# Optimization experiments

Hardware: AMD Instinct MI355X
Metric: run time of the kernel (lower is better)

Reference implementation:

```python
import jax, jax.numpy as jnp
import numpy as np
from jax import lax

STRIDE = 8  # backbone patch-embed stride


def setup_inputs() -> dict:
    key = jax.random.key(0)
    ks = jax.random.split(key, 5)
    B, H, W = 2, 256, 256
    Cr, Cg, Cout = 256, 5, 256
    N = 65536  # memory bank size
    return {
        "image": jax.random.normal(ks[0], (B, 3, H, W), dtype=jnp.float32),
        "geometry_map": jax.random.uniform(ks[1], (B, Cg, H, W), dtype=jnp.float32),
        "backbone_w": jax.random.normal(ks[2], (Cr, 3, STRIDE, STRIDE), dtype=jnp.float32) * 0.05,
        "backbone_b": jnp.zeros((Cr,), dtype=jnp.float32),
        "fusion_w": jax.random.normal(ks[3], (Cout, Cr + Cg), dtype=jnp.float32) * 0.05,
        "fusion_b": jnp.zeros((Cout,), dtype=jnp.float32),
        "memory_bank": jax.random.normal(ks[4], (N, Cout), dtype=jnp.float32),
    }


def reference(image, geometry_map, backbone_w, backbone_b, fusion_w, fusion_b, memory_bank):
    # --- backbone: patch-embed conv + relu -> (B,Cr,H',W') ---
    feat_rgb = lax.conv_general_dilated(
        image, backbone_w, window_strides=(STRIDE, STRIDE), padding="VALID",
        dimension_numbers=("NCHW", "OIHW", "NCHW"))
    feat_rgb = jax.nn.relu(feat_rgb + backbone_b[None, :, None, None])
    B, Cr, H, W = feat_rgb.shape

    # --- bilinear align of geometry map (align_corners=False semantics) ---
    geo = jax.image.resize(geometry_map, (B, geometry_map.shape[1], H, W), method="bilinear")

    # --- fusion 1x1 conv ---
    fused = jnp.concatenate([feat_rgb, geo], axis=1)           # (B, Cr+Cg, H, W)
    fused = jnp.einsum("oc,bchw->bohw", fusion_w, fused) + fusion_b[None, :, None, None]
    C = fused.shape[1]

    # --- NN min-distance to memory bank (cdist + min) ---
    flat = fused.transpose(0, 2, 3, 1).reshape(-1, C)          # (M, C)
    d2 = (jnp.sum(flat * flat, axis=1)[:, None]
          + jnp.sum(memory_bank * memory_bank, axis=1)[None, :]
          - 2.0 * flat @ memory_bank.T)                        # (M, N)
    min_dist = jnp.sqrt(jnp.maximum(jnp.min(d2, axis=1), 0.0))  # sqrt monotone: min before sqrt
    score_plain = min_dist.reshape(B, H, W)

    # --- geometry reweighting (sigmoid mode, alpha=1.0) ---
    density, opacity, anis = geo[:, 3:4], geo[:, 2:3], geo[:, 4:5]
    base = 0.5 * density + 0.25 * (1.0 - opacity) + 0.25 * anis
    w = 1.0 + jax.nn.sigmoid(4.0 * (base - 0.5))               # (B,1,H,W)
    score_geo = score_plain * w[:, 0]
    return score_plain, score_geo
```

## Files before the change

### kernel.cpp

```cpp
#include <hip/hip_runtime.h>
#include <hip/hip_bf16.h>
#include <stdint.h>

typedef __attribute__((ext_vector_type(8))) short bf16x8;
typedef __attribute__((ext_vector_type(4))) float f32x4;

#define NP 2048
#define NBANK 65536
#define NCHUNKS 32
#define CHUNK 2048
#define SUBR 64
#define NSUB 32
#define CF 261

__device__ inline short f2bf(float f) {
  __hip_bfloat16 h = __float2bfloat16(f);
  return *reinterpret_cast<short*>(&h);
}

__global__ __launch_bounds__(256) void k_repack_fw(
    const float* __restrict__ fw, float* __restrict__ fwp)
{
  int idx = blockIdx.x * 256 + threadIdx.x;
  int o = idx / 264, c = idx % 264;
  fwp[idx] = (c < CF) ? fw[(size_t)o * CF + c] : 0.f;
}

__global__ __launch_bounds__(512) void k_prep(
    const float* __restrict__ image, const float* __restrict__ geometry,
    const float* __restrict__ bw, const float* __restrict__ bb,
    const float* __restrict__ fwp, const float* __restrict__ fb,
    const float* __restrict__ mb,
    short* __restrict__ flatb, float* __restrict__ qsq, float* __restrict__ wgt,
    short* __restrict__ mbb, float* __restrict__ msq)
{
  __shared__ __align__(16) unsigned char shmem[32768];
  int t = threadIdx.x;
  int bid = blockIdx.x;

  if (bid >= 256) {
    int s = bid - 256;
    int r = t >> 3, q = t & 7;
    int wcs = r >> 5, hh = (r >> 4) & 1, l15r = r & 15;
    const float* src = mb + ((size_t)s * 64 + r) * 256;
    float s2 = 0.f;
    #pragma unroll
    for (int i = 0; i < 8; i++) {
      float4 v = *(const float4*)(src + q * 4 + i * 32);
      short4 o; o.x = f2bf(v.x); o.y = f2bf(v.y); o.z = f2bf(v.z); o.w = f2bf(v.w);
      int kbyte = q * 8 + i * 64;
      int ks = kbyte >> 6, l4 = (kbyte >> 4) & 3, b8 = kbyte & 8;
      int c = wcs * 16 + hh * 8 + ks;
      *(short4*)(shmem + c * 1024 + l4 * 256 + l15r * 16 + b8) = o;
      s2 += v.x * v.x + v.y * v.y + v.z * v.z + v.w * v.w;
    }
    s2 += __shfl_xor(s2, 1); s2 += __shfl_xor(s2, 2); s2 += __shfl_xor(s2, 4);
    if (q == 0) msq[(size_t)s * 64 + r] = s2;
    __syncthreads();
    unsigned char* dstg = (unsigned char*)mbb + (size_t)s * 32768;
    #pragma unroll
    for (int i = 0; i < 4; i++) {
      int S = t + i * 512;
      *(float4*)(dstg + S * 16) = *(const float4*)(shmem + S * 16);
    }
    return;
  }

  float* patch = (float*)shmem;
  float (*fusedS)[264] = (float (*)[264])(shmem + 6144);
  float (*gv)[8] = (float (*)[8])(shmem + 14592);
  float (*gw)[8] = (float (*)[8])(shmem + 15872);
  float (*redS)[8] = (float (*)[8])(shmem + 17152);

  int b = bid >> 7, rem = bid & 127, h = rem >> 2, w0 = (rem & 3) * 8;

  #pragma unroll
  for (int j = 0; j < 3; j++) {
    int idx = t + j * 512;
    int c = idx >> 9, r = (idx >> 6) & 7, col = idx & 63;
    patch[idx] = image[(((size_t)(b*3 + c) * 256) + 8*h + r) * 256 + 8*w0 + col];
  }
  if (t >= 320 && t < 344) {
    int i = (t - 320) / 3, c = 261 + (t - 320) % 3;
    fusedS[i][c] = 0.f;
  }
  if (t < 320) {
    int v = t >> 3, sub = t & 7;
    int i = v / 5, cg = v % 5;
    int jj = w0 + i;
    float val = 0.f, ws = 0.f;
    const float* gch = geometry + (size_t)(b*5 + cg) * 65536;
    #pragma unroll
    for (int rr = 0; rr < 2; rr++) {
      int r = sub * 2 + rr;
      int gr = 8*h - 4 + r;
      float wr = 1.f - fabsf((float)r - 7.5f) * 0.125f;
      if (gr >= 0 && gr < 256) {
        const float* grow = gch + (size_t)gr * 256;
        for (int c = 0; c < 16; c++) {
          int gc = 8*jj - 4 + c;
          if (gc >= 0 && gc < 256) {
            float wc_ = 1.f - fabsf((float)c - 7.5f) * 0.125f;
            val += wr * wc_ * grow[gc];
            ws  += wr * wc_;
          }
        }
      }
    }
    gv[v][sub] = val; gw[v][sub] = ws;
  }
  __syncthreads();
  if (t < 40) {
    int i = t / 5, cg = t % 5;
    float sv = 0.f, sw = 0.f;
    #pragma unroll
    for (int u = 0; u < 8; u++) { sv += gv[t][u]; sw += gw[t][u]; }
    fusedS[i][256 + cg] = sv / sw;
  }

  int g = t >> 8, o = t & 255;
  float a4[4] = {0.f, 0.f, 0.f, 0.f};
  const float4* wo4 = (const float4*)(bw + (size_t)o * 192);
  for (int cr = 0; cr < 24; cr++) {
    const float4* prow4 = (const float4*)&patch[cr * 64 + g * 32];
    float4 wA = wo4[cr*2], wB = wo4[cr*2 + 1];
    #pragma unroll
    for (int i4 = 0; i4 < 4; i4++) {
      float4 p0 = prow4[i4*2], p1 = prow4[i4*2 + 1];
      a4[i4] += wA.x*p0.x + wA.y*p0.y + wA.z*p0.z + wA.w*p0.w
              + wB.x*p1.x + wB.y*p1.y + wB.z*p1.z + wB.w*p1.w;
    }
  }
  float bias = bb[o];
  #pragma unroll
  for (int i4 = 0; i4 < 4; i4++) fusedS[g*4 + i4][o] = fmaxf(a4[i4] + bias, 0.f);
  __syncthreads();

  #pragma unroll
  for (int i4 = 0; i4 < 4; i4++) a4[i4] = 0.f;
  const float4* fwo4 = (const float4*)(fwp + (size_t)o * 264);
  for (int c4 = 0; c4 < 66; c4++) {
    float4 w4 = fwo4[c4];
    #pragma unroll
    for (int i4 = 0; i4 < 4; i4++) {
      float4 f4 = *(const float4*)&fusedS[g*4 + i4][c4*4];
      a4[i4] += w4.x*f4.x + w4.y*f4.y + w4.z*f4.z + w4.w*f4.w;
    }
  }
  float fbias = fb[o];
  int lane = t & 63, wid = t >> 6;
  #pragma unroll
  for (int i4 = 0; i4 < 4; i4++) {
    a4[i4] += fbias;
    int p = b*1024 + h*32 + w0 + g*4 + i4;
    flatb[(size_t)p * 256 + o] = f2bf(a4[i4]);
    float s = a4[i4] * a4[i4];
    #pragma unroll
    for (int m = 1; m < 64; m <<= 1) s += __shfl_xor(s, m);
    if (lane == 0) redS[g*4 + i4][wid & 3] = s;
  }
  __syncthreads();
  if (t < 8) {
    float s = redS[t][0] + redS[t][1] + redS[t][2] + redS[t][3];
    int p = b*1024 + h*32 + w0 + t;
    qsq[p] = s;
    float den = fusedS[t][256+3], opa = fusedS[t][256+2], ani = fusedS[t][256+4];
    float base2 = 0.5f*den + 0.25f*(1.f - opa) + 0.25f*ani;
    wgt[p] = 1.f + 1.f/(1.f + expf(-4.f*(base2 - 0.5f)));
  }
}

__global__ __launch_bounds__(256, 2) void k_distmin(
    const short* __restrict__ Aq, const short* __restrict__ Bb,
    const float* __restrict__ qsq, const float* __restrict__ msq,
    float* __restrict__ partial)
{
  __shared__ __align__(16) unsigned char sB[2][32768];
  __shared__ float red[2][128];
  int t = threadIdx.x;
  int lane = t & 63, wid = t >> 6;
  int wr = wid >> 1, wc = wid & 1;
  const int l15 = lane & 15, l4 = lane >> 4;
  int nc = blockIdx.x, mt = blockIdx.y;
  int m0 = mt * 128;
  const size_t nchunk0 = (size_t)nc * CHUNK;
  const unsigned char* Bbyte = (const unsigned char*)Bb + nchunk0 * 512;
  const unsigned char* Abyte = (const unsigned char*)Aq;

  bf16x8 af[4][8];
  #pragma unroll
  for (int mi = 0; mi < 4; mi++)
    #pragma unroll
    for (int ks = 0; ks < 8; ks++)
      af[mi][ks] = *(const bf16x8*)(Abyte +
          (size_t)(m0 + wr*64 + mi*16 + l15) * 512 + ks*64 + l4*16);

  float vmin[4][4];
  #pragma unroll
  for (int mi = 0; mi < 4; mi++)
    #pragma unroll
    for (int r = 0; r < 4; r++) vmin[mi][r] = 3.4e38f;

#define STAGE(bufsel, sidx) do {                                              \
    const unsigned char* gb_ = Bbyte + (size_t)(sidx) * 32768 + wid * 1024 + lane * 16; \
    unsigned char* lb_ = &sB[bufsel][0] + wid * 1024;                         \
    _Pragma("unroll")                                                         \
    for (int j_ = 0; j_ < 8; j_++) {                                          \
      __builtin_amdgcn_global_load_lds(                                       \
        (const __attribute__((address_space(1))) unsigned int*)(gb_ + j_*4096), \
        (__attribute__((address_space(3))) unsigned int*)(lb_ + j_*4096),     \
        16, 0, 0);                                                            \
    }                                                                         \
  } while (0)

  STAGE(0, 0);
  __syncthreads();

  int cur = 0;
  for (int s = 0; s < NSUB; s++) {
    if (s + 1 < NSUB) STAGE(cur ^ 1, s + 1);
    const size_t nb = nchunk0 + (size_t)s * SUBR;
    float msq0 = msq[nb + wc * 32 + l15];
    float msq1 = msq[nb + wc * 32 + 16 + l15];
    const unsigned char* buf = &sB[cur][0] + wc * 16384;

    f32x4 acc[4][2];
    #pragma unroll
    for (int mi = 0; mi < 4; mi++) {
      acc[mi][0] = (f32x4){0.f, 0.f, 0.f, 0.f};
      acc[mi][1] = (f32x4){0.f, 0.f, 0.f, 0.f};
    }
    #pragma unroll
    for (int ks = 0; ks < 8; ks++) {
      bf16x8 b0 = *(const bf16x8*)(buf + ks*1024 + l4*256 + l15*16);
      bf16x8 b1 = *(const bf16x8*)(buf + 8192 + ks*1024 + l4*256 + l15*16);
      #pragma unroll
      for (int mi = 0; mi < 4; mi++) {
        acc[mi][0] = __builtin_amdgcn_mfma_f32_16x16x32_bf16(af[mi][ks], b0, acc[mi][0], 0, 0, 0);
        acc[mi][1] = __builtin_amdgcn_mfma_f32_16x16x32_bf16(af[mi][ks], b1, acc[mi][1], 0, 0, 0);
      }
    }
    #pragma unroll
    for (int mi = 0; mi < 4; mi++)
      #pragma unroll
      for (int r = 0; r < 4; r++) {
        float v = fminf(msq0 - 2.f*acc[mi][0][r], msq1 - 2.f*acc[mi][1][r]);
        vmin[mi][r] = fminf(vmin[mi][r], v);
      }
    __syncthreads();
    cur ^= 1;
  }
#undef STAGE

  #pragma unroll
  for (int mi = 0; mi < 4; mi++)
    #pragma unroll
    for (int r = 0; r < 4; r++) {
      float v = vmin[mi][r];
      v = fminf(v, __shfl_xor(v, 1));
      v = fminf(v, __shfl_xor(v, 2));
      v = fminf(v, __shfl_xor(v, 4));
      v = fminf(v, __shfl_xor(v, 8));
      if (l15 == 0) red[wc][wr * 64 + mi * 16 + l4 * 4 + r] = v;
    }
  __syncthreads();
  if (t < 128) {
    float v = fminf(red[0][t], red[1][t]);
    float d2 = qsq[m0 + t] + v;
    partial[(size_t)(m0 + t) * NCHUNKS + nc] = fmaxf(d2, 0.f);
  }
}

__global__ __launch_bounds__(256) void k_final(
    const float* __restrict__ partial, const float* __restrict__ wgt,
    float* __restrict__ out)
{
  int q = blockIdx.x * 256 + threadIdx.x;
  const float4* p = (const float4*)(partial + (size_t)q * NCHUNKS);
  float v = 3.4e38f;
  #pragma unroll
  for (int j = 0; j < 8; j++) {
    float4 x = p[j];
    v = fminf(v, fminf(fminf(x.x, x.y), fminf(x.z, x.w)));
  }
  float sp = sqrtf(v);
  out[q] = sp;
  out[NP + q] = sp * wgt[q];
}

extern "C" void kernel_launch(void* const* d_in, const int* in_sizes, int n_in,
                              void* d_out, int out_size, void* d_ws, size_t ws_size,
                              hipStream_t stream) {
  const float* image    = (const float*)d_in[0];
  const float* geometry = (const float*)d_in[1];
  const float* bw       = (const float*)d_in[2];
  const float* bb       = (const float*)d_in[3];
  const float* fw       = (const float*)d_in[4];
  const float* fb       = (const float*)d_in[5];
  const float* mb       = (const float*)d_in[6];
  float* out = (float*)d_out;
  char* ws = (char*)d_ws;

  float* wgt     = (float*)(ws);
  float* qsq     = (float*)(ws + 8192);
  float* msq     = (float*)(ws + 16384);
  float* fwp     = (float*)(ws + 278528);
  short* flatb   = (short*)(ws + 548864);
  float* partial = (float*)(ws + 1597440);
  short* mbb     = (short*)(ws + 1859584);

  hipLaunchKernelGGL(k_repack_fw, dim3(264),     dim3(256), 0, stream, fw, fwp);
  hipLaunchKernelGGL(k_prep,      dim3(1280),    dim3(512), 0, stream,
                     image, geometry, bw, bb, fwp, fb, mb, flatb, qsq, wgt, mbb, msq);
  hipLaunchKernelGGL(k_distmin,   dim3(32, 16),  dim3(256), 0, stream, flatb, mbb, qsq, msq, partial);
  hipLaunchKernelGGL(k_final,     dim3(8),       dim3(256), 0, stream, partial, wgt, out);
}
```

Measured before the change: 199.2 us.

## Fuse prep, distmin and final stages into one cooperative persistent kernel

Merges the conv/fusion prep, memory-bank repack, distance-min and final reduction into a single cooperative kernel of 512 blocks separated by grid-wide syncs. A strided 2D device memcpy replaces the weight repack kernel. The conv blocks move to 256 threads, each producing all 8 pixels per output channel, and bank repack blocks handle 4 subtiles each. The goal is to remove kernel launch gaps and tail effects between stages. The costs are grid.sync overhead, reduced prep parallelism (512 blocks instead of 1280) and a per-call host occupancy query, with a non-cooperative fallback path kept.

```diff
diff --git a/kernel.cpp b/kernel.cpp
--- a/kernel.cpp
+++ b/kernel.cpp
@@ -1,6 +1,9 @@
 #include <hip/hip_runtime.h>
 #include <hip/hip_bf16.h>
+#include <hip/hip_cooperative_groups.h>
 #include <stdint.h>
+
+namespace cg = cooperative_groups;
 
 typedef __attribute__((ext_vector_type(8))) short bf16x8;
 typedef __attribute__((ext_vector_type(4))) float f32x4;
@@ -18,81 +21,41 @@
   return *reinterpret_cast<short*>(&h);
 }
 
-__global__ __launch_bounds__(256) void k_repack_fw(
-    const float* __restrict__ fw, float* __restrict__ fwp)
-{
-  int idx = blockIdx.x * 256 + threadIdx.x;
-  int o = idx / 264, c = idx % 264;
-  fwp[idx] = (c < CF) ? fw[(size_t)o * CF + c] : 0.f;
-}
-
-__global__ __launch_bounds__(512) void k_prep(
+
+__device__ void conv_block_256(
+    unsigned char* shmem, int bid, int t,
     const float* __restrict__ image, const float* __restrict__ geometry,
     const float* __restrict__ bw, const float* __restrict__ bb,
     const float* __restrict__ fwp, const float* __restrict__ fb,
-    const float* __restrict__ mb,
-    short* __restrict__ flatb, float* __restrict__ qsq, float* __restrict__ wgt,
-    short* __restrict__ mbb, float* __restrict__ msq)
-{
-  __shared__ __align__(16) unsigned char shmem[32768];
-  int t = threadIdx.x;
-  int bid = blockIdx.x;
-
-  if (bid >= 256) {
-    int s = bid - 256;
-    int r = t >> 3, q = t & 7;
-    int wcs = r >> 5, hh = (r >> 4) & 1, l15r = r & 15;
-    const float* src = mb + ((size_t)s * 64 + r) * 256;
-    float s2 = 0.f;
-    #pragma unroll
-    for (int i = 0; i < 8; i++) {
-      float4 v = *(const float4*)(src + q * 4 + i * 32);
-      short4 o; o.x = f2bf(v.x); o.y = f2bf(v.y); o.z = f2bf(v.z); o.w = f2bf(v.w);
-      int kbyte = q * 8 + i * 64;
-      int ks = kbyte >> 6, l4 = (kbyte >> 4) & 3, b8 = kbyte & 8;
-      int c = wcs * 16 + hh * 8 + ks;
-      *(short4*)(shmem + c * 1024 + l4 * 256 + l15r * 16 + b8) = o;
-      s2 += v.x * v.x + v.y * v.y + v.z * v.z + v.w * v.w;
-    }
-    s2 += __shfl_xor(s2, 1); s2 += __shfl_xor(s2, 2); s2 += __shfl_xor(s2, 4);
-    if (q == 0) msq[(size_t)s * 64 + r] = s2;
-    __syncthreads();
-    unsigned char* dstg = (unsigned char*)mbb + (size_t)s * 32768;
-    #pragma unroll
-    for (int i = 0; i < 4; i++) {
-      int S = t + i * 512;
-      *(float4*)(dstg + S * 16) = *(const float4*)(shmem + S * 16);
-    }
-    return;
-  }
-
+    short* __restrict__ flatb, float* __restrict__ qsq, float* __restrict__ wgt)
+{
   float* patch = (float*)shmem;
   float (*fusedS)[264] = (float (*)[264])(shmem + 6144);
-  float (*gv)[8] = (float (*)[8])(shmem + 14592);
-  float (*gw)[8] = (float (*)[8])(shmem + 15872);
-  float (*redS)[8] = (float (*)[8])(shmem + 17152);
+  float (*gv)[4] = (float (*)[4])(shmem + 14592);
+  float (*gw)[4] = (float (*)[4])(shmem + 15232);
+  float (*redS)[8] = (float (*)[8])(shmem + 15872);
 
   int b = bid >> 7, rem = bid & 127, h = rem >> 2, w0 = (rem & 3) * 8;
 
   #pragma unroll
-  for (int j = 0; j < 3; j++) {
-    int idx = t + j * 512;
+  for (int j = 0; j < 6; j++) {
+    int idx = t + j * 256;
     int c = idx >> 9, r = (idx >> 6) & 7, col = idx & 63;
     patch[idx] = image[(((size_t)(b*3 + c) * 256) + 8*h + r) * 256 + 8*w0 + col];
   }
-  if (t >= 320 && t < 344) {
-    int i = (t - 320) / 3, c = 261 + (t - 320) % 3;
+  if (t < 24) {
+    int i = t / 3, c = 261 + t % 3;
     fusedS[i][c] = 0.f;
   }
-  if (t < 320) {
-    int v = t >> 3, sub = t & 7;
-    int i = v / 5, cg = v % 5;
+  if (t < 160) {
+    int v = t >> 2, sub = t & 3;
+    int i = v / 5, cg5 = v % 5;
     int jj = w0 + i;
     float val = 0.f, ws = 0.f;
-    const float* gch = geometry + (size_t)(b*5 + cg) * 65536;
-    #pragma unroll
-    for (int rr = 0; rr < 2; rr++) {
-      int r = sub * 2 + rr;
+    const float* gch = geometry + (size_t)(b*5 + cg5) * 65536;
+    #pragma unroll
+    for (int rr = 0; rr < 4; rr++) {
+      int r = sub * 4 + rr;
       int gr = 8*h - 4 + r;
       float wr = 1.f - fabsf((float)r - 7.5f) * 0.125f;
       if (gr >= 0 && gr < 256) {
@@ -111,57 +74,57 @@
   }
   __syncthreads();
   if (t < 40) {
-    int i = t / 5, cg = t % 5;
-    float sv = 0.f, sw = 0.f;
-    #pragma unroll
-    for (int u = 0; u < 8; u++) { sv += gv[t][u]; sw += gw[t][u]; }
-    fusedS[i][256 + cg] = sv / sw;
-  }
-
-  int g = t >> 8, o = t & 255;
-  float a4[4] = {0.f, 0.f, 0.f, 0.f};
-  const float4* wo4 = (const float4*)(bw + (size_t)o * 192);
+    int i = t / 5, cg5 = t % 5;
+    float sv = gv[t][0] + gv[t][1] + gv[t][2] + gv[t][3];
+    float sw = gw[t][0] + gw[t][1] + gw[t][2] + gw[t][3];
+    fusedS[i][256 + cg5] = sv / sw;
+  }
+
+  float acc[8];
+  #pragma unroll
+  for (int i = 0; i < 8; i++) acc[i] = 0.f;
+  const float4* wo4 = (const float4*)(bw + (size_t)t * 192);
   for (int cr = 0; cr < 24; cr++) {
-    const float4* prow4 = (const float4*)&patch[cr * 64 + g * 32];
+    const float4* prow4 = (const float4*)&patch[cr * 64];
     float4 wA = wo4[cr*2], wB = wo4[cr*2 + 1];
     #pragma unroll
-    for (int i4 = 0; i4 < 4; i4++) {
-      float4 p0 = prow4[i4*2], p1 = prow4[i4*2 + 1];
-      a4[i4] += wA.x*p0.x + wA.y*p0.y + wA.z*p0.z + wA.w*p0.w
+    for (int i = 0; i < 8; i++) {
+      float4 p0 = prow4[i*2], p1 = prow4[i*2 + 1];
+      acc[i] += wA.x*p0.x + wA.y*p0.y + wA.z*p0.z + wA.w*p0.w
               + wB.x*p1.x + wB.y*p1.y + wB.z*p1.z + wB.w*p1.w;
     }
   }
-  float bias = bb[o];
-  #pragma unroll
-  for (int i4 = 0; i4 < 4; i4++) fusedS[g*4 + i4][o] = fmaxf(a4[i4] + bias, 0.f);
-  __syncthreads();
-
-  #pragma unroll
-  for (int i4 = 0; i4 < 4; i4++) a4[i4] = 0.f;
-  const float4* fwo4 = (const float4*)(fwp + (size_t)o * 264);
+  float bias = bb[t];
+  #pragma unroll
+  for (int i = 0; i < 8; i++) fusedS[i][t] = fmaxf(acc[i] + bias, 0.f);
+  __syncthreads();
+
+  #pragma unroll
+  for (int i = 0; i < 8; i++) acc[i] = 0.f;
+  const float4* fwo4 = (const float4*)(fwp + (size_t)t * 264);
   for (int c4 = 0; c4 < 66; c4++) {
     float4 w4 = fwo4[c4];
     #pragma unroll
-    for (int i4 = 0; i4 < 4; i4++) {
-      float4 f4 = *(const float4*)&fusedS[g*4 + i4][c4*4];
-      a4[i4] += w4.x*f4.x + w4.y*f4.y + w4.z*f4.z + w4.w*f4.w;
-    }
-  }
-  float fbias = fb[o];
-  int lane = t & 63, wid = t >> 6;
-  #pragma unroll
-  for (int i4 = 0; i4 < 4; i4++) {
-    a4[i4] += fbias;
-    int p = b*1024 + h*32 + w0 + g*4 + i4;
-    flatb[(size_t)p * 256 + o] = f2bf(a4[i4]);
-    float s = a4[i4] * a4[i4];
+    for (int i = 0; i < 8; i++) {
+      float4 f4 = *(const float4*)&fusedS[i][c4*4];
+      acc[i] += w4.x*f4.x + w4.y*f4.y + w4.z*f4.z + w4.w*f4.w;
+    }
+  }
+  float fbias = fb[t];
+  int lane = t & 63, wvid = t >> 6;
+  #pragma unroll
+  for (int i = 0; i < 8; i++) {
+    acc[i] += fbias;
+    int p = b*1024 + h*32 + w0 + i;
+    flatb[(size_t)p * 256 + t] = f2bf(acc[i]);
+    float s = acc[i] * acc[i];
     #pragma unroll
     for (int m = 1; m < 64; m <<= 1) s += __shfl_xor(s, m);
-    if (lane == 0) redS[g*4 + i4][wid & 3] = s;
+    if (lane == 0) redS[wvid][i] = s;
   }
   __syncthreads();
   if (t < 8) {
-    float s = redS[t][0] + redS[t][1] + redS[t][2] + redS[t][3];
+    float s = redS[0][t] + redS[1][t] + redS[2][t] + redS[3][t];
     int p = b*1024 + h*32 + w0 + t;
     qsq[p] = s;
     float den = fusedS[t][256+3], opa = fusedS[t][256+2], ani = fusedS[t][256+4];
@@ -170,18 +133,50 @@
   }
 }
 
-__global__ __launch_bounds__(256, 2) void k_distmin(
+__device__ void bank_subtile_256(
+    unsigned char* shmem, int s, int t,
+    const float* __restrict__ mb, short* __restrict__ mbb,
+    float* __restrict__ msq)
+{
+  int r = t >> 2, q4 = t & 3;
+  int wcs = r >> 5, hh = (r >> 4) & 1, l15r = r & 15;
+  const float* src = mb + ((size_t)s * 64 + r) * 256;
+  float s2 = 0.f;
+  #pragma unroll
+  for (int qq = q4; qq < 8; qq += 4) {
+    int l4 = (qq >> 1) & 3, b8 = (qq & 1) * 8;
+    #pragma unroll
+    for (int i = 0; i < 8; i++) {
+      float4 v = *(const float4*)(src + qq * 4 + i * 32);
+      short4 o; o.x = f2bf(v.x); o.y = f2bf(v.y); o.z = f2bf(v.z); o.w = f2bf(v.w);
+      int c = wcs * 16 + hh * 8 + i;
+      *(short4*)(shmem + c * 1024 + l4 * 256 + l15r * 16 + b8) = o;
+      s2 += v.x*v.x + v.y*v.y + v.z*v.z + v.w*v.w;
+    }
+  }
+  s2 += __shfl_xor(s2, 1); s2 += __shfl_xor(s2, 2);
+  if (q4 == 0) msq[(size_t)s * 64 + r] = s2;
+  __syncthreads();
+  unsigned char* dstg = (unsigned char*)mbb + (size_t)s * 32768;
+  #pragma unroll
+  for (int i = 0; i < 8; i++) {
+    int S = t + i * 256;
+    *(float4*)(dstg + S * 16) = *(const float4*)(shmem + S * 16);
+  }
+  __syncthreads();
+}
+
+__device__ void distmin_block(
+    unsigned char* shmem, int nc, int mt, int t,
     const short* __restrict__ Aq, const short* __restrict__ Bb,
     const float* __restrict__ qsq, const float* __restrict__ msq,
     float* __restrict__ partial)
 {
-  __shared__ __align__(16) unsigned char sB[2][32768];
-  __shared__ float red[2][128];
-  int t = threadIdx.x;
+  unsigned char (*sB)[32768] = (unsigned char (*)[32768])shmem;
+  float (*red)[128] = (float (*)[128])shmem;
   int lane = t & 63, wid = t >> 6;
   int wr = wid >> 1, wc = wid & 1;
   const int l15 = lane & 15, l4 = lane >> 4;
-  int nc = blockIdx.x, mt = blockIdx.y;
   int m0 = mt * 128;
   const size_t nchunk0 = (size_t)nc * CHUNK;
   const unsigned char* Bbyte = (const unsigned char*)Bb + nchunk0 * 512;
@@ -271,7 +266,79 @@
   }
 }
 
-__global__ __launch_bounds__(256) void k_final(
+__global__ __launch_bounds__(256, 2) void k_fused(
+    const float* __restrict__ image, const float* __restrict__ geometry,
+    const float* __restrict__ bw, const float* __restrict__ bb,
+    const float* __restrict__ fwp, const float* __restrict__ fb,
+    const float* __restrict__ mb,
+    short* __restrict__ flatb, float* __restrict__ qsq, float* __restrict__ wgt,
+    short* __restrict__ mbb, float* __restrict__ msq,
+    float* __restrict__ partial, float* __restrict__ out)
+{
+  __shared__ __align__(16) unsigned char shmem[65536];
+  cg::grid_group grid = cg::this_grid();
+  int t = threadIdx.x;
+  int bid = blockIdx.x;
+
+  if (bid < 256) {
+    conv_block_256(shmem, bid, t, image, geometry, bw, bb, fwp, fb,
+                   flatb, qsq, wgt);
+  } else {
+    for (int ss = 0; ss < 4; ss++)
+      bank_subtile_256(shmem, (bid - 256) * 4 + ss, t, mb, mbb, msq);
+  }
+
+  grid.sync();
+
+  distmin_block(shmem, bid & 31, bid >> 5, t, flatb, mbb, qsq, msq, partial);
+
+  grid.sync();
+
+  if (bid < 8) {
+    int q = bid * 256 + t;
+    const float4* p = (const float4*)(partial + (size_t)q * NCHUNKS);
+    float v = 3.4e38f;
+    #pragma unroll
+    for (int j = 0; j < 8; j++) {
+      float4 x = p[j];
+      v = fminf(v, fminf(fminf(x.x, x.y), fminf(x.z, x.w)));
+    }
+    float sp = sqrtf(v);
+    out[q] = sp;
+    out[NP + q] = sp * wgt[q];
+  }
+}
+
+__global__ __launch_bounds__(256) void k_prep_fb(
+    const float* __restrict__ image, const float* __restrict__ geometry,
+    const float* __restrict__ bw, const float* __restrict__ bb,
+    const float* __restrict__ fwp, const float* __restrict__ fb,
+    const float* __restrict__ mb,
+    short* __restrict__ flatb, float* __restrict__ qsq, float* __restrict__ wgt,
+    short* __restrict__ mbb, float* __restrict__ msq)
+{
+  __shared__ __align__(16) unsigned char shmem[32768];
+  int t = threadIdx.x;
+  int bid = blockIdx.x;
+  if (bid < 256) {
+    conv_block_256(shmem, bid, t, image, geometry, bw, bb, fwp, fb,
+                   flatb, qsq, wgt);
+  } else {
+    bank_subtile_256(shmem, bid - 256, t, mb, mbb, msq);
+  }
+}
+
+__global__ __launch_bounds__(256, 2) void k_distmin_fb(
+    const short* __restrict__ Aq, const short* __restrict__ Bb,
+    const float* __restrict__ qsq, const float* __restrict__ msq,
+    float* __restrict__ partial)
+{
+  __shared__ __align__(16) unsigned char shmem[65536];
+  distmin_block(shmem, blockIdx.x, blockIdx.y, threadIdx.x,
+                Aq, Bb, qsq, msq, partial);
+}
+
+__global__ __launch_bounds__(256) void k_final_fb(
     const float* __restrict__ partial, const float* __restrict__ wgt,
     float* __restrict__ out)
 {
@@ -309,9 +376,34 @@
   float* partial = (float*)(ws + 1597440);
   short* mbb     = (short*)(ws + 1859584);
 
-  hipLaunchKernelGGL(k_repack_fw, dim3(264),     dim3(256), 0, stream, fw, fwp);
-  hipLaunchKernelGGL(k_prep,      dim3(1280),    dim3(512), 0, stream,
-                     image, geometry, bw, bb, fwp, fb, mb, flatb, qsq, wgt, mbb, msq);
-  hipLaunchKernelGGL(k_distmin,   dim3(32, 16),  dim3(256), 0, stream, flatb, mbb, qsq, msq, partial);
-  hipLaunchKernelGGL(k_final,     dim3(8),       dim3(256), 0, stream, partial, wgt, out);
-}
+  hipMemcpy2DAsync(fwp, 264 * sizeof(float), fw, 261 * sizeof(float),
+                   261 * sizeof(float), 256, hipMemcpyDeviceToDevice, stream);
+
+  int coop = 0, occ = 0;
+  hipDeviceGetAttribute(&coop, hipDeviceAttributeCooperativeLaunch, 0);
+  hipOccupancyMaxActiveBlocksPerMultiprocessor(&occ, (const void*)k_fused, 256, 0);
+
+  bool launched = false;
+  if (coop && occ >= 2) {
+    void* args[] = {
+      (void*)&image, (void*)&geometry, (void*)&bw, (void*)&bb, (void*)&fwp,
+      (void*)&fb, (void*)&mb, (void*)&flatb, (void*)&qsq, (void*)&wgt,
+      (void*)&mbb, (void*)&msq, (void*)&partial, (void*)&out
+    };
+    hipError_t err = hipLaunchCooperativeKernel((const void*)k_fused,
+                                                dim3(512), dim3(256),
+                                                args, 0, stream);
+    launched = (err == hipSuccess);
+    if (!launched) (void)hipGetLastError();
+  }
+
+  if (!launched) {
+    hipLaunchKernelGGL(k_prep_fb,    dim3(1280),   dim3(256), 0, stream,
+                       image, geometry, bw, bb, fwp, fb, mb,
+                       flatb, qsq, wgt, mbb, msq);
+    hipLaunchKernelGGL(k_distmin_fb, dim3(32, 16), dim3(256), 0, stream,
+                       flatb, mbb, qsq, msq, partial);
+    hipLaunchKernelGGL(k_final_fb,   dim3(8),      dim3(256), 0, stream,
+                       partial, wgt, out);
+  }
+}
```

Result: slower. 230.5 us (+15.7%).
